# Kernel optimization log

Hardware: AMD Instinct MI355X
Metric: run time of the kernel (lower is better)

Reference implementation:

```python
import jax, jax.numpy as jnp
import numpy as np

N_NODES = 50000


def gcn_conv(x, src, dst, norm, W, b, n_nodes):
    """One GCNConv layer: out = scatter_add(norm * (x @ W)[src] -> dst) + b.
    src/dst already include self loops; norm is the symmetric D^-1/2 A_hat D^-1/2 edge weight."""
    h = x @ W  # [N, C_out]
    msg = h[src] * norm[:, None]  # [E+N, C_out]
    out = jax.ops.segment_sum(msg, dst, num_segments=n_nodes)
    return out + b


def build_norm(edge_index, n_nodes):
    """Add self loops and compute symmetric GCN normalization (PyG GCNConv default)."""
    loop = jnp.arange(n_nodes, dtype=edge_index.dtype)
    src = jnp.concatenate([edge_index[0], loop])
    dst = jnp.concatenate([edge_index[1], loop])
    deg = jax.ops.segment_sum(jnp.ones_like(dst, dtype=jnp.float32), dst, num_segments=n_nodes)
    dinv = jnp.where(deg > 0, jax.lax.rsqrt(jnp.maximum(deg, 1.0)), 0.0)
    norm = dinv[src] * dinv[dst]
    return src, dst, norm


def setup_inputs() -> dict:
    key = jax.random.key(0)
    ks = jax.random.split(key, 8)
    in_c, h1, h2, out_c = 768, 256, 128, 2
    x = jax.random.normal(ks[0], (N_NODES, in_c), dtype=jnp.float32)
    edge_index = jax.random.randint(ks[1], (2, 800000), 0, N_NODES, dtype=jnp.int32)
    W1 = jax.random.normal(ks[2], (in_c, h1), dtype=jnp.float32) * 0.02
    b1 = jnp.zeros((h1,), dtype=jnp.float32)
    W2 = jax.random.normal(ks[3], (h1, h2), dtype=jnp.float32) * 0.02
    b2 = jnp.zeros((h2,), dtype=jnp.float32)
    W3 = jax.random.normal(ks[4], (h2, out_c), dtype=jnp.float32) * 0.02
    b3 = jnp.zeros((out_c,), dtype=jnp.float32)
    return {"x": x, "edge_index": edge_index, "W1": W1, "b1": b1,
            "W2": W2, "b2": b2, "W3": W3, "b3": b3}


def reference(x, edge_index, W1, b1, W2, b2, W3, b3):
    n = x.shape[0]
    src, dst, norm = build_norm(edge_index, n)
    # Dropout is identity in eval mode (training=False), so it is omitted.
    h = jax.nn.relu(gcn_conv(x, src, dst, norm, W1, b1, n))
    h = jax.nn.relu(gcn_conv(h, src, dst, norm, W2, b2, n))
    h = gcn_conv(h, src, dst, norm, W3, b3, n)
    return jax.nn.sigmoid(h)
```

## Files before the change

kernel.cpp:

```cpp
#include <hip/hip_runtime.h>
#include <math.h>

typedef short s16x8 __attribute__((ext_vector_type(8)));
typedef __bf16 b16x8 __attribute__((ext_vector_type(8)));
typedef float f32x4 __attribute__((ext_vector_type(4)));
typedef float f32x2 __attribute__((ext_vector_type(2)));
typedef unsigned int u32x4 __attribute__((ext_vector_type(4)));
typedef unsigned int u32x2 __attribute__((ext_vector_type(2)));

__device__ inline short f2bf(float f) {
    unsigned u = __float_as_uint(f);
    unsigned r = u + 0x7FFFu + ((u >> 16) & 1u);
    return (short)(r >> 16);
}


__global__ void count_kernel(const int* __restrict__ dst, int* __restrict__ cnt, int E) {
    int e = blockIdx.x * 256 + threadIdx.x;
    if (e < E) atomicAdd(&cnt[dst[e]], 1);
}


__device__ inline void make_wt_elem(const float* __restrict__ W, short* __restrict__ Wt,
                                    int K, int N, int idx) {
    int NB = N >> 7;
    int j = idx & 7;
    int l = (idx >> 3) & 63;
    int nt = (idx >> 9) & 7;
    int rest = idx >> 12;
    int b = rest % NB;
    int c = rest / NB;
    int k = c * 32 + (l >> 4) * 8 + j;
    int n = b * 128 + nt * 16 + (l & 15);
    Wt[idx] = f2bf(W[(size_t)k * N + n]);
}

__global__ __launch_bounds__(1024) void scanfix_kernel(
        const int* __restrict__ cnt, int* __restrict__ rp, int* __restrict__ cursor,
        float* __restrict__ dinv, int* __restrict__ bsum, int n, int E, int SB,
        const float* __restrict__ W1, short* __restrict__ Wt1,
        const float* __restrict__ W2, short* __restrict__ Wt2, int w1b) {
    int tid = threadIdx.x;
    if (blockIdx.x >= SB) {
        int b = blockIdx.x - SB;
        if (b < w1b) {
            int idx = b * 1024 + tid;
            make_wt_elem(W1, Wt1, 768, 256, idx);
        } else {
            int idx = (b - w1b) * 1024 + tid;
            make_wt_elem(W2, Wt2, 256, 128, idx);
        }
        return;
    }

    __shared__ int sdata[1024];
    __shared__ int parts[64];
    __shared__ int carry_s;
    int i = blockIdx.x * 1024 + tid;
    int v = (i < n) ? cnt[i] : 0;
    sdata[tid] = v;
    __syncthreads();
    for (int off = 1; off < 1024; off <<= 1) {
        int t = 0;
        if (tid >= off) t = sdata[tid - off];
        __syncthreads();
        sdata[tid] += t;
        __syncthreads();
    }
    if (tid == 1023)
        __hip_atomic_store(&bsum[blockIdx.x], sdata[1023] + 1,
                           __ATOMIC_RELEASE, __HIP_MEMORY_SCOPE_AGENT);
    int part = 0;
    if (tid < blockIdx.x) {
        int b;
        while ((b = __hip_atomic_load(&bsum[tid], __ATOMIC_ACQUIRE,
                                      __HIP_MEMORY_SCOPE_AGENT)) == 0) {}
        part = b - 1;
    }
    if (tid < 64) parts[tid] = part;
    __syncthreads();
    if (tid == 0) {
        int c = 0;
        for (int k = 0; k < 64; ++k) c += parts[k];
        carry_s = c;
    }
    __syncthreads();
    int r = sdata[tid] - v + carry_s;
    if (i < n) {
        rp[i] = r;
        cursor[i] = r;
        dinv[i] = rsqrtf((float)cnt[i] + 1.0f);
    }
    if (i == 0) rp[n] = E;
}


__global__ __launch_bounds__(256, 3) void gemm1_fill_kernel(
        const float* __restrict__ x, const short* __restrict__ Wt,
        unsigned char* __restrict__ h8, int M, int G1B, int FB,
        const int* __restrict__ src, const int* __restrict__ dst,
        int* __restrict__ cursor, const float* __restrict__ dinv,
        int2* __restrict__ ecw, int E) {
    constexpr int KC = 24;
    constexpr int RT = 2;
    constexpr int O = KC * 4;
    constexpr int F = KC * RT * 64 / 256;

    __shared__ s16x8 As[KC * RT * 64];

    const int tid = threadIdx.x;
    const int total = G1B + FB;
    const long long bi = (long long)blockIdx.x;
    const int fid  = (int)(bi * FB / total);
    const int fid1 = (int)((bi + 1) * FB / total);

    if (fid1 > fid) {
        int e = fid * 256 + tid;
        if (e < E) {
            int d = dst[e];
            int s = src[e];
            int p = atomicAdd(&cursor[d], 1);
            ecw[p] = make_int2(s, __float_as_int(dinv[s] * dinv[d]));
        }
        return;
    }
    const int gid = blockIdx.x - fid;

    const int m0 = gid * (RT * 16);

    s16x8 v[F];
#pragma unroll
    for (int i = 0; i < F; ++i) {
        int idx = i * 256 + tid;
        int r = idx / O;
        int o = idx - r * O;
        int row = m0 + r;
        if (row >= M) row = M - 1;
        const float4* fp = (const float4*)(x + (size_t)row * 768 + o * 8);
        float4 f0 = fp[0];
        float4 f1 = fp[1];
        u32x4 pk;
        pk.x = (__float_as_uint(f0.x) >> 16) | (__float_as_uint(f0.y) & 0xFFFF0000u);
        pk.y = (__float_as_uint(f0.z) >> 16) | (__float_as_uint(f0.w) & 0xFFFF0000u);
        pk.z = (__float_as_uint(f1.x) >> 16) | (__float_as_uint(f1.y) & 0xFFFF0000u);
        pk.w = (__float_as_uint(f1.z) >> 16) | (__float_as_uint(f1.w) & 0xFFFF0000u);
        v[i] = __builtin_bit_cast(s16x8, pk);
    }
#pragma unroll
    for (int i = 0; i < F; ++i) {
        int idx = i * 256 + tid;
        int r = idx / O;
        int o = idx - r * O;
        int c = o >> 2, q = o & 3;
        int slot = q * 16 + (((r & 15) + q + ((c & 3) << 2)) & 15);
        As[(c * RT + (r >> 4)) * 64 + slot] = v[i];
    }
    __syncthreads();

    const int lane = tid & 63;
    const int wave = tid >> 6;
    const int b128 = wave >> 1;
    const int nt0 = (wave & 1) * 4;
    const int q = lane >> 4;
    const int rl = lane & 15;
    const s16x8* wt = (const s16x8*)Wt;

    f32x4 acc[RT][4];
#pragma unroll
    for (int i = 0; i < RT; ++i)
#pragma unroll
        for (int j = 0; j < 4; ++j)
            acc[i][j] = (f32x4){0.f, 0.f, 0.f, 0.f};

#pragma unroll 4
    for (int c = 0; c < KC; ++c) {
        int slot = q * 16 + ((rl + q + ((c & 3) << 2)) & 15);
        b16x8 areg[RT], breg[4];
#pragma unroll
        for (int i = 0; i < RT; ++i)
            areg[i] = __builtin_bit_cast(b16x8, As[(c * RT + i) * 64 + slot]);
        size_t bb = (size_t)(c * 2 + b128) * 512 + nt0 * 64 + lane;
#pragma unroll
        for (int j = 0; j < 4; ++j)
            breg[j] = __builtin_bit_cast(b16x8, wt[bb + j * 64]);
#pragma unroll
        for (int i = 0; i < RT; ++i)
#pragma unroll
            for (int j = 0; j < 4; ++j)
                acc[i][j] = __builtin_amdgcn_mfma_f32_16x16x32_bf16(areg[i], breg[j], acc[i][j], 0, 0, 0);
    }

    const int quad = lane >> 4;
    const int nl = lane & 15;
#pragma unroll
    for (int i = 0; i < RT; ++i) {
        int rbase = m0 + i * 16 + quad * 4;
#pragma unroll
        for (int j = 0; j < 4; ++j) {
            int col = wave * 64 + j * 16 + nl;
#pragma unroll
            for (int r = 0; r < 4; ++r) {
                int row = rbase + r;
                if (row < M) {
                    unsigned u = __builtin_amdgcn_cvt_pk_fp8_f32(acc[i][j][r], acc[i][j][r], 0, false);
                    h8[(size_t)row * 256 + col] = (unsigned char)(u & 0xFF);
                }
            }
        }
    }
}


__global__ __launch_bounds__(256) void agg256_g2_kernel(const unsigned char* __restrict__ h8,
                                                        const int* __restrict__ rp,
                                                        const int2* __restrict__ ecw,
                                                        const float* __restrict__ dinv,
                                                        const float* __restrict__ bias,
                                                        const short* __restrict__ Wt2,
                                                        unsigned char* __restrict__ h2, int n) {
    __shared__ s16x8 As[8 * 64];

    const int tid = threadIdx.x;
    const int lane = tid & 63;
    const int wave = tid >> 6;
    const int eg = lane >> 4;
    const int ch = lane & 15;
    const int nb0 = blockIdx.x * 16;

    for (int t = 0; t < 4; ++t) {
        const int r = wave * 4 + t;
        const int node = nb0 + r;
        float acc[16];
#pragma unroll
        for (int k = 0; k < 16; ++k) acc[k] = 0.f;

        if (node < n) {
            float di = dinv[node];
            {
                u32x4 v = *(const u32x4*)(h8 + (size_t)node * 256 + ch * 16);
                float ws = (eg == 0) ? di * di : 0.f;
#pragma unroll
                for (int u = 0; u < 4; ++u) {
                    f32x2 lo = __builtin_amdgcn_cvt_pk_f32_fp8(v[u], false);
                    f32x2 hi = __builtin_amdgcn_cvt_pk_f32_fp8(v[u], true);
                    acc[u * 4 + 0] = ws * lo.x; acc[u * 4 + 1] = ws * lo.y;
                    acc[u * 4 + 2] = ws * hi.x; acc[u * 4 + 3] = ws * hi.y;
                }
            }
            int e0 = rp[node], e1 = rp[node + 1];
            for (int base = e0; base < e1; base += 64) {
                int idx = base + lane;
                int2 er = (idx < e1) ? ecw[idx] : make_int2(0, 0);
                int sb = er.x;
                float wb = __int_as_float(er.y);
                int cnt = e1 - base; if (cnt > 64) cnt = 64;
#pragma unroll 4
                for (int i = 0; i < cnt; i += 4) {
                    int s = __shfl(sb, i + eg, 64);
                    float w = __shfl(wb, i + eg, 64);
                    u32x4 v = *(const u32x4*)(h8 + (size_t)s * 256 + ch * 16);
#pragma unroll
                    for (int u = 0; u < 4; ++u) {
                        f32x2 lo = __builtin_amdgcn_cvt_pk_f32_fp8(v[u], false);
                        f32x2 hi = __builtin_amdgcn_cvt_pk_f32_fp8(v[u], true);
                        acc[u * 4 + 0] += w * lo.x; acc[u * 4 + 1] += w * lo.y;
                        acc[u * 4 + 2] += w * hi.x; acc[u * 4 + 3] += w * hi.y;
                    }
                }
            }
#pragma unroll
            for (int k = 0; k < 16; ++k) {
                acc[k] += __shfl_xor(acc[k], 16, 64);
                acc[k] += __shfl_xor(acc[k], 32, 64);
            }
#pragma unroll
            for (int k = 0; k < 16; ++k)
                acc[k] = fmaxf(acc[k] + bias[ch * 16 + k], 0.f);
        }

        if (eg < 2) {
            s16x8 v;
            int base = eg * 8;
#pragma unroll
            for (int k = 0; k < 8; ++k) v[k] = f2bf(acc[base + k]);
            int o = 2 * ch + eg;
            int c = o >> 2, q = o & 3;
            int slot = q * 16 + ((r + q + ((c & 3) << 2)) & 15);
            As[c * 64 + slot] = v;
        }
    }
    __syncthreads();

    const int q = lane >> 4;
    const int rl = lane & 15;
    const s16x8* wt = (const s16x8*)Wt2;

    f32x4 acc2[2];
    acc2[0] = (f32x4){0.f, 0.f, 0.f, 0.f};
    acc2[1] = (f32x4){0.f, 0.f, 0.f, 0.f};

#pragma unroll
    for (int c = 0; c < 8; ++c) {
        int slot = q * 16 + ((rl + q + ((c & 3) << 2)) & 15);
        b16x8 areg = __builtin_bit_cast(b16x8, As[c * 64 + slot]);
        size_t bb = (size_t)c * 512 + (wave * 2) * 64 + lane;
        b16x8 b0 = __builtin_bit_cast(b16x8, wt[bb]);
        b16x8 b1 = __builtin_bit_cast(b16x8, wt[bb + 64]);
        acc2[0] = __builtin_amdgcn_mfma_f32_16x16x32_bf16(areg, b0, acc2[0], 0, 0, 0);
        acc2[1] = __builtin_amdgcn_mfma_f32_16x16x32_bf16(areg, b1, acc2[1], 0, 0, 0);
    }

    const int quad = lane >> 4;
    const int nl = lane & 15;
#pragma unroll
    for (int j = 0; j < 2; ++j) {
        int col = (wave * 2 + j) * 16 + nl;
#pragma unroll
        for (int rr = 0; rr < 4; ++rr) {
            int row = nb0 + quad * 4 + rr;
            if (row < n) {
                unsigned u = __builtin_amdgcn_cvt_pk_fp8_f32(acc2[j][rr], acc2[j][rr], 0, false);
                h2[(size_t)row * 128 + col] = (unsigned char)(u & 0xFF);
            }
        }
    }
}

__global__ __launch_bounds__(256) void agg128_w3_kernel(const unsigned char* __restrict__ h,
                                                        const int* __restrict__ rp,
                                                        const int2* __restrict__ ecw,
                                                        const float* __restrict__ dinv,
                                                        const float* __restrict__ b2,
                                                        const float* __restrict__ W3,
                                                        float* __restrict__ z, int n) {
    int node = blockIdx.x * 4 + (threadIdx.x >> 6);
    int lane = threadIdx.x & 63;
    if (node >= n) return;
    const int eg = lane >> 4;
    const int ch = lane & 15;
    float di = dinv[node];

    float acc[8];
    {
        u32x2 v = *(const u32x2*)(h + (size_t)node * 128 + ch * 8);
        float ws = (eg == 0) ? di * di : 0.f;
        f32x2 l0 = __builtin_amdgcn_cvt_pk_f32_fp8(v.x, false);
        f32x2 h0 = __builtin_amdgcn_cvt_pk_f32_fp8(v.x, true);
        f32x2 l1 = __builtin_amdgcn_cvt_pk_f32_fp8(v.y, false);
        f32x2 h1 = __builtin_amdgcn_cvt_pk_f32_fp8(v.y, true);
        acc[0] = ws * l0.x; acc[1] = ws * l0.y; acc[2] = ws * h0.x; acc[3] = ws * h0.y;
        acc[4] = ws * l1.x; acc[5] = ws * l1.y; acc[6] = ws * h1.x; acc[7] = ws * h1.y;
    }

    int e0 = rp[node], e1 = rp[node + 1];
    for (int base = e0; base < e1; base += 64) {
        int idx = base + lane;
        int2 er = (idx < e1) ? ecw[idx] : make_int2(0, 0);
        int sb = er.x;
        float wb = __int_as_float(er.y);
        int cnt = e1 - base; if (cnt > 64) cnt = 64;
#pragma unroll 4
        for (int i = 0; i < cnt; i += 4) {
            int s = __shfl(sb, i + eg, 64);
            float w = __shfl(wb, i + eg, 64);
            u32x2 v = *(const u32x2*)(h + (size_t)s * 128 + ch * 8);
            f32x2 l0 = __builtin_amdgcn_cvt_pk_f32_fp8(v.x, false);
            f32x2 h0 = __builtin_amdgcn_cvt_pk_f32_fp8(v.x, true);
            f32x2 l1 = __builtin_amdgcn_cvt_pk_f32_fp8(v.y, false);
            f32x2 h1 = __builtin_amdgcn_cvt_pk_f32_fp8(v.y, true);
            acc[0] += w * l0.x; acc[1] += w * l0.y; acc[2] += w * h0.x; acc[3] += w * h0.y;
            acc[4] += w * l1.x; acc[5] += w * l1.y; acc[6] += w * h1.x; acc[7] += w * h1.y;
        }
    }

#pragma unroll
    for (int k = 0; k < 8; ++k) {
        acc[k] += __shfl_xor(acc[k], 16, 64);
        acc[k] += __shfl_xor(acc[k], 32, 64);
    }

    float z0 = 0.f, z1 = 0.f;
#pragma unroll
    for (int k = 0; k < 8; ++k) {
        float a = fmaxf(acc[k] + b2[ch * 8 + k], 0.f);
        z0 += a * W3[(ch * 8 + k) * 2];
        z1 += a * W3[(ch * 8 + k) * 2 + 1];
    }
    for (int off = 8; off > 0; off >>= 1) {
        z0 += __shfl_xor(z0, off, 64);
        z1 += __shfl_xor(z1, off, 64);
    }
    if (lane == 0) {
        z[2 * (size_t)node] = z0;
        z[2 * (size_t)node + 1] = z1;
    }
}

__global__ __launch_bounds__(256) void agg3_kernel(const float* __restrict__ z,
                                                   const int* __restrict__ rp,
                                                   const int2* __restrict__ ecw,
                                                   const float* __restrict__ dinv,
                                                   const float* __restrict__ bias,
                                                   float* __restrict__ out, int n) {
    int node = blockIdx.x * 4 + (threadIdx.x >> 6);
    int lane = threadIdx.x & 63;
    if (node >= n) return;
    float a0 = 0.f, a1 = 0.f;
    int e0 = rp[node], e1 = rp[node + 1];
    for (int idx = e0 + lane; idx < e1; idx += 64) {
        int2 er = ecw[idx];
        float w = __int_as_float(er.y);
        float2 zz = *(const float2*)(z + 2 * (size_t)er.x);
        a0 += w * zz.x;
        a1 += w * zz.y;
    }
    for (int off = 32; off > 0; off >>= 1) {
        a0 += __shfl_xor(a0, off, 64);
        a1 += __shfl_xor(a1, off, 64);
    }
    if (lane == 0) {
        float di = dinv[node];
        float2 zn = *(const float2*)(z + 2 * (size_t)node);
        a0 += di * di * zn.x + bias[0];
        a1 += di * di * zn.y + bias[1];
        out[2 * (size_t)node]     = 1.f / (1.f + __expf(-a0));
        out[2 * (size_t)node + 1] = 1.f / (1.f + __expf(-a1));
    }
}


extern "C" void kernel_launch(void* const* d_in, const int* in_sizes, int n_in,
                              void* d_out, int out_size, void* d_ws, size_t ws_size,
                              hipStream_t stream) {
    const float* x  = (const float*)d_in[0];
    const int*   ei = (const int*)d_in[1];
    const float* W1 = (const float*)d_in[2];
    const float* b1 = (const float*)d_in[3];
    const float* W2 = (const float*)d_in[4];
    const float* b2 = (const float*)d_in[5];
    const float* W3 = (const float*)d_in[6];
    const float* b3 = (const float*)d_in[7];
    float* out = (float*)d_out;

    const int E  = in_sizes[1] / 2;
    const int C1 = in_sizes[3];
    const int C2 = in_sizes[5];
    const int K1 = in_sizes[2] / C1;
    const int N  = in_sizes[0] / K1;

    const int* srcv = ei;
    const int* dstv = ei + E;

    char* p = (char*)d_ws;
    auto carve = [&](size_t bytes) {
        char* r = p;
        p += (bytes + 255) & ~(size_t)255;
        return r;
    };
    int*   cnt    = (int*)carve((size_t)N * 4);
    int*   bsum   = (int*)carve(1024 * 4);
    int*   rp     = (int*)carve((size_t)(N + 1) * 4);
    int*   cursor = (int*)carve((size_t)N * 4);
    float* dinv   = (float*)carve((size_t)N * 4);
    int2*  ecw    = (int2*)carve((size_t)E * 8);
    short* Wt1    = (short*)carve((size_t)K1 * C1 * 2);
    short* Wt2    = (short*)carve((size_t)C1 * C2 * 2);
    unsigned char* h8 = (unsigned char*)carve((size_t)N * C1);
    unsigned char* h2 = (unsigned char*)carve((size_t)N * C2);
    float* zbuf   = (float*)carve((size_t)N * 2 * 4);

    const int nb  = (N + 1023) / 1024;
    const int cb  = (E + 255) / 256;
    const int w1b = (K1 * C1) / 1024;
    const int w2b = (C1 * C2) / 1024;
    const int g1b = (N + 31) / 32;
    const int fb  = (E + 255) / 256;

    size_t cntpad = (((size_t)N * 4) + 255) & ~(size_t)255;
    hipMemsetAsync(cnt, 0, cntpad + 1024 * 4, stream);
    count_kernel<<<cb, 256, 0, stream>>>(dstv, cnt, E);
    scanfix_kernel<<<nb + w1b + w2b, 1024, 0, stream>>>(cnt, rp, cursor, dinv, bsum,
                                                        N, E, nb, W1, Wt1, W2, Wt2, w1b);

    gemm1_fill_kernel<<<g1b + fb, 256, 0, stream>>>(x, Wt1, h8, N, g1b, fb,
                                                    srcv, dstv, cursor, dinv, ecw, E);

    agg256_g2_kernel<<<(N + 15) / 16, 256, 0, stream>>>(h8, rp, ecw, dinv, b1, Wt2, h2, N);

    agg128_w3_kernel<<<(N + 3) / 4, 256, 0, stream>>>(h2, rp, ecw, dinv, b2, W3, zbuf, N);

    agg3_kernel<<<(N + 3) / 4, 256, 0, stream>>>(zbuf, rp, ecw, dinv, b3, out, N);
}
```

Measured before the change: 419.3 us.

## Use one wave per node in fused layer-1 aggregation with 1024-thread blocks

```diff
diff --git a/kernel.cpp b/kernel.cpp
--- a/kernel.cpp
+++ b/kernel.cpp
@@ -211,13 +211,11 @@
 }
 
 
-__global__ __launch_bounds__(256) void agg256_g2_kernel(const unsigned char* __restrict__ h8,
-                                                        const int* __restrict__ rp,
-                                                        const int2* __restrict__ ecw,
-                                                        const float* __restrict__ dinv,
-                                                        const float* __restrict__ bias,
-                                                        const short* __restrict__ Wt2,
-                                                        unsigned char* __restrict__ h2, int n) {
+__global__ __launch_bounds__(1024, 8) void agg256_g2_kernel(
+        const unsigned char* __restrict__ h8, const int* __restrict__ rp,
+        const int2* __restrict__ ecw, const float* __restrict__ dinv,
+        const float* __restrict__ bias, const short* __restrict__ Wt2,
+        unsigned char* __restrict__ h2, int n) {
     __shared__ s16x8 As[8 * 64];
 
     const int tid = threadIdx.x;
@@ -226,102 +224,91 @@
     const int eg = lane >> 4;
     const int ch = lane & 15;
     const int nb0 = blockIdx.x * 16;
-
-    for (int t = 0; t < 4; ++t) {
-        const int r = wave * 4 + t;
-        const int node = nb0 + r;
-        float acc[16];
-#pragma unroll
-        for (int k = 0; k < 16; ++k) acc[k] = 0.f;
-
-        if (node < n) {
-            float di = dinv[node];
-            {
-                u32x4 v = *(const u32x4*)(h8 + (size_t)node * 256 + ch * 16);
-                float ws = (eg == 0) ? di * di : 0.f;
+    const int node = nb0 + wave;
+
+    float acc[16];
+#pragma unroll
+    for (int k = 0; k < 16; ++k) acc[k] = 0.f;
+
+    if (node < n) {
+        float di = dinv[node];
+        {
+            u32x4 v = *(const u32x4*)(h8 + (size_t)node * 256 + ch * 16);
+            float ws = (eg == 0) ? di * di : 0.f;
+#pragma unroll
+            for (int u = 0; u < 4; ++u) {
+                f32x2 lo = __builtin_amdgcn_cvt_pk_f32_fp8(v[u], false);
+                f32x2 hi = __builtin_amdgcn_cvt_pk_f32_fp8(v[u], true);
+                acc[u * 4 + 0] = ws * lo.x; acc[u * 4 + 1] = ws * lo.y;
+                acc[u * 4 + 2] = ws * hi.x; acc[u * 4 + 3] = ws * hi.y;
+            }
+        }
+        int e0 = rp[node], e1 = rp[node + 1];
+        for (int base = e0; base < e1; base += 64) {
+            int idx = base + lane;
+            int2 er = (idx < e1) ? ecw[idx] : make_int2(0, 0);
+            int sb = er.x;
+            float wb = __int_as_float(er.y);
+            int cnt = e1 - base; if (cnt > 64) cnt = 64;
+#pragma unroll 4
+            for (int i = 0; i < cnt; i += 4) {
+                int s = __shfl(sb, i + eg, 64);
+                float w = __shfl(wb, i + eg, 64);
+                u32x4 v = *(const u32x4*)(h8 + (size_t)s * 256 + ch * 16);
 #pragma unroll
                 for (int u = 0; u < 4; ++u) {
                     f32x2 lo = __builtin_amdgcn_cvt_pk_f32_fp8(v[u], false);
                     f32x2 hi = __builtin_amdgcn_cvt_pk_f32_fp8(v[u], true);
-                    acc[u * 4 + 0] = ws * lo.x; acc[u * 4 + 1] = ws * lo.y;
-                    acc[u * 4 + 2] = ws * hi.x; acc[u * 4 + 3] = ws * hi.y;
+                    acc[u * 4 + 0] += w * lo.x; acc[u * 4 + 1] += w * lo.y;
+                    acc[u * 4 + 2] += w * hi.x; acc[u * 4 + 3] += w * hi.y;
                 }
             }
-            int e0 = rp[node], e1 = rp[node + 1];
-            for (int base = e0; base < e1; base += 64) {
-                int idx = base + lane;
-                int2 er = (idx < e1) ? ecw[idx] : make_int2(0, 0);
-                int sb = er.x;
-                float wb = __int_as_float(er.y);
-                int cnt = e1 - base; if (cnt > 64) cnt = 64;
-#pragma unroll 4
-                for (int i = 0; i < cnt; i += 4) {
-                    int s = __shfl(sb, i + eg, 64);
-                    float w = __shfl(wb, i + eg, 64);
-                    u32x4 v = *(const u32x4*)(h8 + (size_t)s * 256 + ch * 16);
-#pragma unroll
-                    for (int u = 0; u < 4; ++u) {
-                        f32x2 lo = __builtin_amdgcn_cvt_pk_f32_fp8(v[u], false);
-                        f32x2 hi = __builtin_amdgcn_cvt_pk_f32_fp8(v[u], true);
-                        acc[u * 4 + 0] += w * lo.x; acc[u * 4 + 1] += w * lo.y;
-                        acc[u * 4 + 2] += w * hi.x; acc[u * 4 + 3] += w * hi.y;
-                    }
-                }
-            }
-#pragma unroll
-            for (int k = 0; k < 16; ++k) {
-                acc[k] += __shfl_xor(acc[k], 16, 64);
-                acc[k] += __shfl_xor(acc[k], 32, 64);
-            }
-#pragma unroll
-            for (int k = 0; k < 16; ++k)
-                acc[k] = fmaxf(acc[k] + bias[ch * 16 + k], 0.f);
-        }
-
-        if (eg < 2) {
-            s16x8 v;
-            int base = eg * 8;
-#pragma unroll
-            for (int k = 0; k < 8; ++k) v[k] = f2bf(acc[base + k]);
-            int o = 2 * ch + eg;
-            int c = o >> 2, q = o & 3;
-            int slot = q * 16 + ((r + q + ((c & 3) << 2)) & 15);
-            As[c * 64 + slot] = v;
-        }
+        }
+#pragma unroll
+        for (int k = 0; k < 16; ++k) {
+            acc[k] += __shfl_xor(acc[k], 16, 64);
+            acc[k] += __shfl_xor(acc[k], 32, 64);
+        }
+#pragma unroll
+        for (int k = 0; k < 16; ++k)
+            acc[k] = fmaxf(acc[k] + bias[ch * 16 + k], 0.f);
+    }
+
+    if (eg < 2) {
+        s16x8 v;
+        int base = eg * 8;
+#pragma unroll
+        for (int k = 0; k < 8; ++k) v[k] = f2bf(acc[base + k]);
+        int o = 2 * ch + eg;
+        int c = o >> 2, q = o & 3;
+        int slot = q * 16 + ((wave + q + ((c & 3) << 2)) & 15);
+        As[c * 64 + slot] = v;
     }
     __syncthreads();
 
+    if (wave >= 8) return;
     const int q = lane >> 4;
     const int rl = lane & 15;
     const s16x8* wt = (const s16x8*)Wt2;
 
-    f32x4 acc2[2];
-    acc2[0] = (f32x4){0.f, 0.f, 0.f, 0.f};
-    acc2[1] = (f32x4){0.f, 0.f, 0.f, 0.f};
-
+    f32x4 acc2 = (f32x4){0.f, 0.f, 0.f, 0.f};
 #pragma unroll
     for (int c = 0; c < 8; ++c) {
         int slot = q * 16 + ((rl + q + ((c & 3) << 2)) & 15);
         b16x8 areg = __builtin_bit_cast(b16x8, As[c * 64 + slot]);
-        size_t bb = (size_t)c * 512 + (wave * 2) * 64 + lane;
-        b16x8 b0 = __builtin_bit_cast(b16x8, wt[bb]);
-        b16x8 b1 = __builtin_bit_cast(b16x8, wt[bb + 64]);
-        acc2[0] = __builtin_amdgcn_mfma_f32_16x16x32_bf16(areg, b0, acc2[0], 0, 0, 0);
-        acc2[1] = __builtin_amdgcn_mfma_f32_16x16x32_bf16(areg, b1, acc2[1], 0, 0, 0);
+        b16x8 breg = __builtin_bit_cast(b16x8, wt[(size_t)c * 512 + wave * 64 + lane]);
+        acc2 = __builtin_amdgcn_mfma_f32_16x16x32_bf16(areg, breg, acc2, 0, 0, 0);
     }
 
     const int quad = lane >> 4;
     const int nl = lane & 15;
-#pragma unroll
-    for (int j = 0; j < 2; ++j) {
-        int col = (wave * 2 + j) * 16 + nl;
-#pragma unroll
-        for (int rr = 0; rr < 4; ++rr) {
-            int row = nb0 + quad * 4 + rr;
-            if (row < n) {
-                unsigned u = __builtin_amdgcn_cvt_pk_fp8_f32(acc2[j][rr], acc2[j][rr], 0, false);
-                h2[(size_t)row * 128 + col] = (unsigned char)(u & 0xFF);
-            }
+    int col = wave * 16 + nl;
+#pragma unroll
+    for (int rr = 0; rr < 4; ++rr) {
+        int row = nb0 + quad * 4 + rr;
+        if (row < n) {
+            unsigned u = __builtin_amdgcn_cvt_pk_fp8_f32(acc2[rr], acc2[rr], 0, false);
+            h2[(size_t)row * 128 + col] = (unsigned char)(u & 0xFF);
         }
     }
 }
@@ -485,7 +472,7 @@
     gemm1_fill_kernel<<<g1b + fb, 256, 0, stream>>>(x, Wt1, h8, N, g1b, fb,
                                                     srcv, dstv, cursor, dinv, ecw, E);
 
-    agg256_g2_kernel<<<(N + 15) / 16, 256, 0, stream>>>(h8, rp, ecw, dinv, b1, Wt2, h2, N);
+    agg256_g2_kernel<<<(N + 15) / 16, 1024, 0, stream>>>(h8, rp, ecw, dinv, b1, Wt2, h2, N);
 
     agg128_w3_kernel<<<(N + 3) / 4, 256, 0, stream>>>(h2, rp, ecw, dinv, b2, W3, zbuf, N);
 
```

Result: no change. 413.0 us (-1.5%).
